# Optimization experiments

Measured on AMD Instinct MI355X. Metric: run time of the kernel, lower is better.

## Reference

```python
import jax, jax.numpy as jnp
import numpy as np

B, S, H, DH = 64, 64, 64, 64  # S == H == DH required by the module's (buggy) shape logic
D = H * DH  # d_feature = 4096


def setup_inputs() -> dict:
    key = jax.random.key(0)
    ks = jax.random.split(key, 9)
    sc = 1.0 / np.sqrt(D).astype(np.float32)
    return {
        "x": jax.random.normal(ks[0], (B, S, D), jnp.float32),
        "Wq": jax.random.normal(ks[1], (D, D), jnp.float32) * sc,
        "bq": jax.random.normal(ks[2], (D,), jnp.float32) * 0.01,
        "Wk": jax.random.normal(ks[3], (D, D), jnp.float32) * sc,
        "bk": jax.random.normal(ks[4], (D,), jnp.float32) * 0.01,
        "Wv": jax.random.normal(ks[5], (D, D), jnp.float32) * sc,
        "bv": jax.random.normal(ks[6], (D,), jnp.float32) * 0.01,
        "Wp": jax.random.normal(ks[7], (D, D), jnp.float32) * sc,
        "bp": jax.random.normal(ks[8], (D,), jnp.float32) * 0.01,
    }


def reference(x, Wq, bq, Wk, bk, Wv, bv, Wp, bp):
    b, s, d = x.shape
    # nn.Linear: y = x @ W^T + b
    q = (x @ Wq.T + bq).reshape(b, s, H, DH)  # _split's permute(0,1,2,3) is identity
    k = (x @ Wk.T + bk).reshape(b, s, H, DH)
    v = (x @ Wv.T + bv).reshape(b, s, H, DH)
    # scores over HEAD axis (per token), shape (b, S, H, H); scale by sqrt(d_k)=sqrt(DH)
    scores = jnp.einsum("bshd,bsed->bshe", q, k) / np.sqrt(DH).astype(np.float32)
    attn = jax.nn.softmax(scores, axis=-1)
    # attn @ V^T : out[b,s,i,j] = sum_k attn[b,s,i,k] * v[b,s,j,k]  (needs H == DH)
    vals = jnp.einsum("bsik,bsjk->bsij", attn, v)  # (b, S, H, H)
    # _merge: permute(0,2,1,3) -> (b, H, S, H), view(b, H, S*H); S*H == d_feature
    merged = jnp.transpose(vals, (0, 2, 1, 3)).reshape(b, H, s * H)
    return merged @ Wp.T + bp  # (b, H, d_feature)
```

## Files before the change

kernel.cpp:

```cpp
#include <hip/hip_runtime.h>

typedef __attribute__((ext_vector_type(8))) __bf16 bf16x8;
typedef __attribute__((ext_vector_type(4))) float f32x4;

__device__ __forceinline__ float bf2f(unsigned short u) {
    union { unsigned u; float f; } c; c.u = ((unsigned)u) << 16; return c.f;
}
__device__ __forceinline__ unsigned short f2bf(float f) {
    union { float f; unsigned u; } c; c.f = f;
    unsigned r = c.u + 0x7fffu + ((c.u >> 16) & 1u);
    return (unsigned short)(r >> 16);
}

#define GLD_LDS16(g, l) \
    __builtin_amdgcn_global_load_lds( \
        (const __attribute__((address_space(1))) void*)(g), \
        (__attribute__((address_space(3))) void*)(l), 16, 0, 0)

__global__ void __launch_bounds__(256) cvt_f32_bf16(
    const float* __restrict__ s0, unsigned short* __restrict__ d0,
    const float* __restrict__ s1, unsigned short* __restrict__ d1,
    const float* __restrict__ s2, unsigned short* __restrict__ d2,
    const float* __restrict__ s3, unsigned short* __restrict__ d3)
{
    const float* s; unsigned short* d;
    if (blockIdx.z == 0)      { s = s0; d = d0; }
    else if (blockIdx.z == 1) { s = s1; d = d1; }
    else if (blockIdx.z == 2) { s = s2; d = d2; }
    else                      { s = s3; d = d3; }
    const size_t N = (size_t)4096 * 4096;
    const size_t stride = (size_t)gridDim.x * 256 * 4;
    for (size_t i = ((size_t)blockIdx.x * 256 + threadIdx.x) * 4; i < N; i += stride) {
        float4 v = *(const float4*)(s + i);
        ushort4 o;
        o.x = f2bf(v.x); o.y = f2bf(v.y); o.z = f2bf(v.z); o.w = f2bf(v.w);
        *(ushort4*)(d + i) = o;
    }
}

template <bool OUTF32>
__global__ void __launch_bounds__(256) gemm_bt(
    const unsigned short* __restrict__ A,
    const unsigned short* __restrict__ W0, const float* __restrict__ b0, void* __restrict__ C0,
    const unsigned short* __restrict__ W1, const float* __restrict__ b1, void* __restrict__ C1,
    const unsigned short* __restrict__ W2, const float* __restrict__ b2, void* __restrict__ C2)
{
    constexpr int K = 4096;
    const unsigned short* W; const float* bias; void* C;
    if (blockIdx.z == 0)      { W = W0; bias = b0; C = C0; }
    else if (blockIdx.z == 1) { W = W1; bias = b1; C = C1; }
    else                      { W = W2; bias = b2; C = C2; }

    __shared__ __align__(16) unsigned short sA[128 * 32];
    __shared__ __align__(16) unsigned short sB[128 * 32];

    const int tid  = threadIdx.x;
    const int lane = tid & 63;
    const int wave = tid >> 6;
    const int wm = wave >> 1;
    const int wn = wave & 1;
    const int m0 = blockIdx.y * 128;
    const int n0 = blockIdx.x * 128;

    const int srow = lane >> 2;
    const int scol = (lane & 3) << 3;
    const unsigned short* gA0 = A + (size_t)(m0 + wave * 16 + srow) * K + scol;
    const unsigned short* gA1 = gA0 + (size_t)64 * K;
    const unsigned short* gB0 = W + (size_t)(n0 + wave * 16 + srow) * K + scol;
    const unsigned short* gB1 = gB0 + (size_t)64 * K;
    unsigned short* lA0 = &sA[wave * 512];
    unsigned short* lA1 = &sA[(wave + 4) * 512];
    unsigned short* lB0 = &sB[wave * 512];
    unsigned short* lB1 = &sB[(wave + 4) * 512];

    f32x4 acc[4][4];
#pragma unroll
    for (int i = 0; i < 4; i++)
#pragma unroll
        for (int j = 0; j < 4; j++) acc[i][j] = (f32x4){0.f, 0.f, 0.f, 0.f};

    const int fl = lane & 15;
    const int fk = (lane >> 4) << 3;
    const unsigned short* aP0 = &sA[(wm * 64 + fl) * 32 + fk];
    const unsigned short* bP0 = &sB[(wn * 64 + fl) * 32 + fk];

    for (int k0 = 0; k0 < K; k0 += 32) {
        __syncthreads();
        GLD_LDS16(gA0 + k0, lA0);
        GLD_LDS16(gA1 + k0, lA1);
        GLD_LDS16(gB0 + k0, lB0);
        GLD_LDS16(gB1 + k0, lB1);
        __syncthreads();

        bf16x8 af[4], bfr[4];
#pragma unroll
        for (int i = 0; i < 4; i++) af[i]  = *(const bf16x8*)(aP0 + i * 512);
#pragma unroll
        for (int j = 0; j < 4; j++) bfr[j] = *(const bf16x8*)(bP0 + j * 512);
#pragma unroll
        for (int i = 0; i < 4; i++)
#pragma unroll
            for (int j = 0; j < 4; j++)
                acc[i][j] = __builtin_amdgcn_mfma_f32_16x16x32_bf16(af[i], bfr[j], acc[i][j], 0, 0, 0);
    }

    const int r0 = (lane >> 4) << 2;
#pragma unroll
    for (int j = 0; j < 4; j++) {
        const int col = n0 + wn * 64 + j * 16 + fl;
        const float bj = bias[col];
#pragma unroll
        for (int i = 0; i < 4; i++) {
            const int row = m0 + wm * 64 + i * 16 + r0;
#pragma unroll
            for (int r = 0; r < 4; r++) {
                const float val = acc[i][j][r] + bj;
                if constexpr (OUTF32)
                    ((float*)C)[(size_t)(row + r) * 4096 + col] = val;
                else
                    ((unsigned short*)C)[(size_t)(row + r) * 4096 + col] = f2bf(val);
            }
        }
    }
}

__global__ void __launch_bounds__(256) attn_mfma(
    const unsigned short* __restrict__ q, const unsigned short* __restrict__ k,
    const unsigned short* __restrict__ v, unsigned short* __restrict__ merged)
{
    __shared__ __align__(16) unsigned short sP[4][64 * 72];

    const int tid  = threadIdx.x;
    const int wave = tid >> 6;
    const int lane = tid & 63;
    const int token = blockIdx.x * 4 + wave;
    const int b = token >> 6, s = token & 63;
    const size_t base = (size_t)token * 4096;

    const int fl = lane & 15;
    const int qg = lane >> 4;

    f32x4 S[4][4];
#pragma unroll
    for (int i = 0; i < 4; i++)
#pragma unroll
        for (int j = 0; j < 4; j++) S[i][j] = (f32x4){0.f, 0.f, 0.f, 0.f};

#pragma unroll
    for (int ks = 0; ks < 2; ks++) {
        bf16x8 aq[4], bk[4];
#pragma unroll
        for (int t = 0; t < 4; t++) {
            aq[t] = *(const bf16x8*)(q + base + (size_t)(t * 16 + fl) * 64 + ks * 32 + qg * 8);
            bk[t] = *(const bf16x8*)(k + base + (size_t)(t * 16 + fl) * 64 + ks * 32 + qg * 8);
        }
#pragma unroll
        for (int i = 0; i < 4; i++)
#pragma unroll
            for (int j = 0; j < 4; j++)
                S[i][j] = __builtin_amdgcn_mfma_f32_16x16x32_bf16(aq[i], bk[j], S[i][j], 0, 0, 0);
    }

    float mrow[4][4];
#pragma unroll
    for (int i = 0; i < 4; i++)
#pragma unroll
        for (int r = 0; r < 4; r++) {
            float m = S[i][0][r];
            m = fmaxf(m, S[i][1][r]); m = fmaxf(m, S[i][2][r]); m = fmaxf(m, S[i][3][r]);
            mrow[i][r] = m;
        }
#pragma unroll
    for (int off = 1; off <= 8; off <<= 1)
#pragma unroll
        for (int i = 0; i < 4; i++)
#pragma unroll
            for (int r = 0; r < 4; r++)
                mrow[i][r] = fmaxf(mrow[i][r], __shfl_xor(mrow[i][r], off));

    float lrow[4][4];
#pragma unroll
    for (int i = 0; i < 4; i++)
#pragma unroll
        for (int r = 0; r < 4; r++) lrow[i][r] = 0.f;
#pragma unroll
    for (int i = 0; i < 4; i++)
#pragma unroll
        for (int j = 0; j < 4; j++)
#pragma unroll
            for (int r = 0; r < 4; r++) {
                const float p = __expf((S[i][j][r] - mrow[i][r]) * 0.125f);
                S[i][j][r] = p;
                lrow[i][r] += p;
            }
#pragma unroll
    for (int off = 1; off <= 8; off <<= 1)
#pragma unroll
        for (int i = 0; i < 4; i++)
#pragma unroll
            for (int r = 0; r < 4; r++)
                lrow[i][r] += __shfl_xor(lrow[i][r], off);

    unsigned short* myP = &sP[wave][0];
#pragma unroll
    for (int i = 0; i < 4; i++)
#pragma unroll
        for (int r = 0; r < 4; r++) {
            const float inv = 1.f / lrow[i][r];
            const int row = i * 16 + qg * 4 + r;
#pragma unroll
            for (int j = 0; j < 4; j++)
                myP[row * 72 + j * 16 + fl] = f2bf(S[i][j][r] * inv);
        }

    f32x4 O[4][4];
#pragma unroll
    for (int i = 0; i < 4; i++)
#pragma unroll
        for (int j = 0; j < 4; j++) O[i][j] = (f32x4){0.f, 0.f, 0.f, 0.f};

#pragma unroll
    for (int ks = 0; ks < 2; ks++) {
        bf16x8 ap[4], bv[4];
#pragma unroll
        for (int t = 0; t < 4; t++) {
            ap[t] = *(const bf16x8*)(myP + (t * 16 + fl) * 72 + ks * 32 + qg * 8);
            bv[t] = *(const bf16x8*)(v + base + (size_t)(t * 16 + fl) * 64 + ks * 32 + qg * 8);
        }
#pragma unroll
        for (int i = 0; i < 4; i++)
#pragma unroll
            for (int j = 0; j < 4; j++)
                O[i][j] = __builtin_amdgcn_mfma_f32_16x16x32_bf16(ap[i], bv[j], O[i][j], 0, 0, 0);
    }

#pragma unroll
    for (int i = 0; i < 4; i++)
#pragma unroll
        for (int r = 0; r < 4; r++) {
            const size_t rowbase = (size_t)(b * 64 + i * 16 + qg * 4 + r) * 4096 + s * 64;
#pragma unroll
            for (int j = 0; j < 4; j++)
                merged[rowbase + j * 16 + fl] = f2bf(O[i][j][r]);
        }
}

extern "C" void kernel_launch(void* const* d_in, const int* in_sizes, int n_in,
                              void* d_out, int out_size, void* d_ws, size_t ws_size,
                              hipStream_t stream)
{
    const float* x  = (const float*)d_in[0];
    const float* Wq = (const float*)d_in[1];
    const float* bq = (const float*)d_in[2];
    const float* Wk = (const float*)d_in[3];
    const float* bk = (const float*)d_in[4];
    const float* Wv = (const float*)d_in[5];
    const float* bv = (const float*)d_in[6];
    const float* Wp = (const float*)d_in[7];
    const float* bp = (const float*)d_in[8];
    float* out = (float*)d_out;

    const size_t MAT = (size_t)4096 * 4096;
    unsigned short* sw = (unsigned short*)d_ws;
    unsigned short* xb     = sw + 0 * MAT;
    unsigned short* Wqb    = sw + 1 * MAT;
    unsigned short* Wkb    = sw + 2 * MAT;
    unsigned short* Wvb    = sw + 3 * MAT;
    unsigned short* q      = sw + 4 * MAT;
    unsigned short* k      = sw + 5 * MAT;
    unsigned short* v      = sw + 6 * MAT;
    unsigned short* merged = xb;
    unsigned short* Wpb    = Wqb;

    cvt_f32_bf16<<<dim3(2048, 1, 4), 256, 0, stream>>>(x, xb, Wq, Wqb, Wk, Wkb, Wv, Wvb);
    gemm_bt<false><<<dim3(32, 32, 3), 256, 0, stream>>>(
        xb, Wqb, bq, q, Wkb, bk, k, Wvb, bv, v);
    cvt_f32_bf16<<<dim3(2048, 1, 1), 256, 0, stream>>>(Wp, Wpb, Wp, Wpb, Wp, Wpb, Wp, Wpb);
    attn_mfma<<<dim3(1024), 256, 0, stream>>>(q, k, v, merged);
    gemm_bt<true><<<dim3(32, 32, 1), 256, 0, stream>>>(
        merged, Wpb, bp, out, Wpb, bp, out, Wpb, bp, out);
}
```

Baseline: 970.5 us.

## Replace 128x128 GEMM with 256x256 double-buffered swizzled-LDS pipelined GEMM

Swaps the simple 128x128 single-buffered GEMM for a 256x256 tile kernel with 8 waves, 64-wide K steps and 128KB of dynamic LDS. Global-to-LDS loads are double-buffered and interleaved with MFMA quarter-blocks using explicit barriers, waitcnt and setprio. An XOR swizzle is meant to avoid LDS bank conflicts. The larger tile raises reuse per loaded byte and hides load latency, but only 256 blocks go to the output projection, so occupancy and tail effects may suffer.

Result: faster. 791.6 us (-18.4%).

```diff
diff --git a/kernel.cpp b/kernel.cpp
--- a/kernel.cpp
+++ b/kernel.cpp
@@ -39,81 +39,127 @@
 }
 
 template <bool OUTF32>
-__global__ void __launch_bounds__(256) gemm_bt(
+__global__ void __launch_bounds__(512, 2) gemm256(
     const unsigned short* __restrict__ A,
     const unsigned short* __restrict__ W0, const float* __restrict__ b0, void* __restrict__ C0,
     const unsigned short* __restrict__ W1, const float* __restrict__ b1, void* __restrict__ C1,
     const unsigned short* __restrict__ W2, const float* __restrict__ b2, void* __restrict__ C2)
 {
     constexpr int K = 4096;
+    constexpr int NT = 64;
+    extern __shared__ char smem[];
+
     const unsigned short* W; const float* bias; void* C;
     if (blockIdx.z == 0)      { W = W0; bias = b0; C = C0; }
     else if (blockIdx.z == 1) { W = W1; bias = b1; C = C1; }
     else                      { W = W2; bias = b2; C = C2; }
 
-    __shared__ __align__(16) unsigned short sA[128 * 32];
-    __shared__ __align__(16) unsigned short sB[128 * 32];
-
     const int tid  = threadIdx.x;
     const int lane = tid & 63;
     const int wave = tid >> 6;
-    const int wm = wave >> 1;
-    const int wn = wave & 1;
-    const int m0 = blockIdx.y * 128;
-    const int n0 = blockIdx.x * 128;
-
-    const int srow = lane >> 2;
-    const int scol = (lane & 3) << 3;
-    const unsigned short* gA0 = A + (size_t)(m0 + wave * 16 + srow) * K + scol;
-    const unsigned short* gA1 = gA0 + (size_t)64 * K;
-    const unsigned short* gB0 = W + (size_t)(n0 + wave * 16 + srow) * K + scol;
-    const unsigned short* gB1 = gB0 + (size_t)64 * K;
-    unsigned short* lA0 = &sA[wave * 512];
-    unsigned short* lA1 = &sA[(wave + 4) * 512];
-    unsigned short* lB0 = &sB[wave * 512];
-    unsigned short* lB1 = &sB[(wave + 4) * 512];
-
-    f32x4 acc[4][4];
-#pragma unroll
-    for (int i = 0; i < 4; i++)
+    const int wm = wave >> 2;
+    const int wn = wave & 3;
+    const int m0 = blockIdx.y * 256;
+    const int n0 = blockIdx.x * 256;
+
+    const int p = tid << 4;
+    const int o = p ^ (((p >> 9) & 1) << 5);
+    const int srow = ((o >> 11) << 4) | ((o >> 6) & 15);
+    const int scol = (((o >> 10) & 1) << 5) | ((o & 63) >> 1);
+    const unsigned short* pA = A + (size_t)(m0 + srow) * K + scol;
+    const unsigned short* pB = W + (size_t)(n0 + srow) * K + scol;
+
+    const int fl = lane & 15;
+    const int qg = lane >> 4;
+    int rdoff = (fl << 6) + (qg << 4);
+    rdoff ^= (fl & 8) << 2;
+    const int aOffc = (wm << 14) + rdoff;
+    const int bOffc = 32768 + ((wn >> 1) << 14) + ((wn & 1) << 13) + rdoff;
+
+    f32x4 acc[8][4];
+#pragma unroll
+    for (int i = 0; i < 8; i++)
 #pragma unroll
         for (int j = 0; j < 4; j++) acc[i][j] = (f32x4){0.f, 0.f, 0.f, 0.f};
 
-    const int fl = lane & 15;
-    const int fk = (lane >> 4) << 3;
-    const unsigned short* aP0 = &sA[(wm * 64 + fl) * 32 + fk];
-    const unsigned short* bP0 = &sB[(wn * 64 + fl) * 32 + fk];
-
-    for (int k0 = 0; k0 < K; k0 += 32) {
-        __syncthreads();
-        GLD_LDS16(gA0 + k0, lA0);
-        GLD_LDS16(gA1 + k0, lA1);
-        GLD_LDS16(gB0 + k0, lB0);
-        GLD_LDS16(gB1 + k0, lB1);
-        __syncthreads();
-
-        bf16x8 af[4], bfr[4];
-#pragma unroll
-        for (int i = 0; i < 4; i++) af[i]  = *(const bf16x8*)(aP0 + i * 512);
-#pragma unroll
-        for (int j = 0; j < 4; j++) bfr[j] = *(const bf16x8*)(bP0 + j * 512);
-#pragma unroll
-        for (int i = 0; i < 4; i++)
-#pragma unroll
-            for (int j = 0; j < 4; j++)
-                acc[i][j] = __builtin_amdgcn_mfma_f32_16x16x32_bf16(af[i], bfr[j], acc[i][j], 0, 0, 0);
+    bf16x8 af[4][2], bfr0[2][2], bfr1[2][2];
+
+#define STAGE_A(tt, h, bb) do { \
+    GLD_LDS16(pA + (size_t)(tt) * 64 + (size_t)(h) * 524288, \
+              smem + (bb) * 65536 + (h) * 16384 + (wave << 10)); \
+    GLD_LDS16(pA + (size_t)(tt) * 64 + (size_t)(h) * 524288 + 262144, \
+              smem + (bb) * 65536 + (h) * 16384 + 8192 + (wave << 10)); \
+} while (0)
+#define STAGE_B(tt, h, bb) do { \
+    GLD_LDS16(pB + (size_t)(tt) * 64 + (size_t)(h) * 524288, \
+              smem + (bb) * 65536 + 32768 + (h) * 16384 + (wave << 10)); \
+    GLD_LDS16(pB + (size_t)(tt) * 64 + (size_t)(h) * 524288 + 262144, \
+              smem + (bb) * 65536 + 32768 + (h) * 16384 + 8192 + (wave << 10)); \
+} while (0)
+
+#define RD_A(mh, bb) do { \
+    _Pragma("unroll") for (int it_ = 0; it_ < 4; ++it_) \
+    _Pragma("unroll") for (int kk_ = 0; kk_ < 2; ++kk_) \
+        af[it_][kk_] = *(const bf16x8*)(smem + (bb) * 65536 + aOffc + (mh) * 8192 + it_ * 2048 + kk_ * 1024); \
+} while (0)
+#define RD_B(nh, dst, bb) do { \
+    _Pragma("unroll") for (int jt_ = 0; jt_ < 2; ++jt_) \
+    _Pragma("unroll") for (int kk_ = 0; kk_ < 2; ++kk_) \
+        dst[jt_][kk_] = *(const bf16x8*)(smem + (bb) * 65536 + bOffc + (nh) * 4096 + jt_ * 2048 + kk_ * 1024); \
+} while (0)
+
+#define MM(mh, nh, bset) do { \
+    __builtin_amdgcn_s_setprio(1); \
+    _Pragma("unroll") for (int it_ = 0; it_ < 4; ++it_) \
+    _Pragma("unroll") for (int jt_ = 0; jt_ < 2; ++jt_) \
+    _Pragma("unroll") for (int kk_ = 0; kk_ < 2; ++kk_) \
+        acc[(mh) * 4 + it_][(nh) * 2 + jt_] = __builtin_amdgcn_mfma_f32_16x16x32_bf16( \
+            af[it_][kk_], bset[jt_][kk_], acc[(mh) * 4 + it_][(nh) * 2 + jt_], 0, 0, 0); \
+    __builtin_amdgcn_s_setprio(0); \
+} while (0)
+
+#define BAR() __builtin_amdgcn_s_barrier()
+
+    STAGE_A(0, 0, 0); STAGE_A(0, 1, 0);
+    STAGE_B(0, 0, 0); STAGE_B(0, 1, 0);
+    STAGE_B(1, 0, 1); STAGE_B(1, 1, 1);
+    asm volatile("s_waitcnt vmcnt(4)" ::: "memory");
+    BAR();
+    __builtin_amdgcn_sched_barrier(0);
+
+#define TILE(t, bb) do { \
+    RD_A(0, bb); RD_B(0, bfr0, bb); \
+    if ((t) + 1 < NT) STAGE_A((t) + 1, 0, (bb) ^ 1); \
+    BAR(); MM(0, 0, bfr0); BAR(); \
+    RD_B(1, bfr1, bb); \
+    if ((t) + 1 < NT) STAGE_A((t) + 1, 1, (bb) ^ 1); \
+    BAR(); MM(0, 1, bfr1); BAR(); \
+    RD_A(1, bb); \
+    if ((t) + 2 < NT) STAGE_B((t) + 2, 0, (bb)); \
+    BAR(); MM(1, 0, bfr0); BAR(); \
+    if ((t) + 2 < NT) STAGE_B((t) + 2, 1, (bb)); \
+    BAR(); MM(1, 1, bfr1); \
+    if ((t) + 2 < NT) { asm volatile("s_waitcnt vmcnt(4)" ::: "memory"); } \
+    else              { asm volatile("s_waitcnt vmcnt(0)" ::: "memory"); } \
+    BAR(); \
+    __builtin_amdgcn_sched_barrier(0); \
+} while (0)
+
+    for (int t = 0; t < NT; t += 2) {
+        TILE(t, 0);
+        TILE(t + 1, 1);
     }
 
     const int r0 = (lane >> 4) << 2;
 #pragma unroll
-    for (int j = 0; j < 4; j++) {
+    for (int j = 0; j < 4; ++j) {
         const int col = n0 + wn * 64 + j * 16 + fl;
         const float bj = bias[col];
 #pragma unroll
-        for (int i = 0; i < 4; i++) {
-            const int row = m0 + wm * 64 + i * 16 + r0;
-#pragma unroll
-            for (int r = 0; r < 4; r++) {
+        for (int i = 0; i < 8; ++i) {
+            const int row = m0 + wm * 128 + i * 16 + r0;
+#pragma unroll
+            for (int r = 0; r < 4; ++r) {
                 const float val = acc[i][j][r] + bj;
                 if constexpr (OUTF32)
                     ((float*)C)[(size_t)(row + r) * 4096 + col] = val;
@@ -122,6 +168,13 @@
             }
         }
     }
+#undef TILE
+#undef BAR
+#undef MM
+#undef RD_B
+#undef RD_A
+#undef STAGE_B
+#undef STAGE_A
 }
 
 __global__ void __launch_bounds__(256) attn_mfma(
@@ -272,11 +325,20 @@
     unsigned short* merged = xb;
     unsigned short* Wpb    = Wqb;
 
+    static bool attr_done = false;
+    if (!attr_done) {
+        hipFuncSetAttribute(reinterpret_cast<const void*>(gemm256<false>),
+                            hipFuncAttributeMaxDynamicSharedMemorySize, 131072);
+        hipFuncSetAttribute(reinterpret_cast<const void*>(gemm256<true>),
+                            hipFuncAttributeMaxDynamicSharedMemorySize, 131072);
+        attr_done = true;
+    }
+
     cvt_f32_bf16<<<dim3(2048, 1, 4), 256, 0, stream>>>(x, xb, Wq, Wqb, Wk, Wkb, Wv, Wvb);
-    gemm_bt<false><<<dim3(32, 32, 3), 256, 0, stream>>>(
+    gemm256<false><<<dim3(16, 16, 3), 512, 131072, stream>>>(
         xb, Wqb, bq, q, Wkb, bk, k, Wvb, bv, v);
     cvt_f32_bf16<<<dim3(2048, 1, 1), 256, 0, stream>>>(Wp, Wpb, Wp, Wpb, Wp, Wpb, Wp, Wpb);
     attn_mfma<<<dim3(1024), 256, 0, stream>>>(q, k, v, merged);
-    gemm_bt<true><<<dim3(32, 32, 1), 256, 0, stream>>>(
+    gemm256<true><<<dim3(16, 16, 1), 512, 131072, stream>>>(
         merged, Wpb, bp, out, Wpb, bp, out, Wpb, bp, out);
 }
```
